# Optimization experiments

Measured on AMD Instinct MI355X. Metric: run time of the kernel, lower is better.

Reference implementation:

```python
import jax, jax.numpy as jnp
import numpy as np

B, T, D, U = 32, 512, 256, 1024

def setup_inputs() -> dict:
    key = jax.random.key(0)
    ks = jax.random.split(key, 5)
    return {
        "X_vecs": jax.random.normal(ks[0], (B, D), dtype=jnp.float32),
        "X_ts": jax.random.normal(ks[1], (B, T, D), dtype=jnp.float32),
        "mat_A_0": jax.random.normal(ks[2], (D, U), dtype=jnp.float32) * (1.0 / np.sqrt(D)),
        "vec_b_0": jnp.zeros((1, U), dtype=jnp.float32),
        "mat_A_s": jax.random.normal(ks[3], (D, U), dtype=jnp.float32) * (1.0 / np.sqrt(D)),
        "vec_b_s": jnp.zeros((1, U), dtype=jnp.float32),
        "mat_W_d": jax.random.normal(ks[4], (D, U), dtype=jnp.float32) * (1.0 / np.sqrt(D)),
        "vec_b_d": jnp.zeros((1, U), dtype=jnp.float32),
    }

def reference(X_vecs, X_ts, mat_A_0, vec_b_0, mat_A_s, vec_b_s, mat_W_d, vec_b_d):
    softsign = jax.nn.soft_sign  # x / (1 + |x|), the layer's main_activation
    # Learned initial state: H_0 = softsign(X_vecs @ A_0 + b_0)   [B, U]
    H0 = softsign(X_vecs @ mat_A_0 + vec_b_0)
    # Static per-step drive from the vector input (computed once, reused each t)
    drive = X_vecs @ mat_A_s + vec_b_s + vec_b_d  # [B, U]
    # Batched projection of the whole timeseries (one big GEMM instead of T small ones)
    XW = jnp.einsum('btd,du->btu', X_ts, mat_W_d)  # [B, T, U]
    def step(h, x_t):  # h: [B,U], x_t: [B,U]
        h_new = softsign(h + drive + x_t)
        return h_new, h_new
    _, outs = jax.lax.scan(step, H0, jnp.swapaxes(XW, 0, 1))  # outs: [T, B, U]
    return jnp.swapaxes(outs, 0, 1)  # return_sequences=True -> [B, T, U]
```

## Files before the change

kernel.cpp:

```cpp
#include <hip/hip_runtime.h>

#define B_DIM 32
#define T_DIM 512
#define D_DIM 256
#define U_DIM 1024
#define M_DIM (B_DIM * T_DIM)

typedef __bf16 bf16_t;
typedef bf16_t bf16x8 __attribute__((ext_vector_type(8)));
typedef float f32x4 __attribute__((ext_vector_type(4)));

__device__ __forceinline__ float ssign(float z) {
    return z * __builtin_amdgcn_rcpf(1.0f + __builtin_fabsf(z));
}

__global__ __launch_bounds__(256) void prep(const float* __restrict__ Wd,
                                            bf16_t* __restrict__ Wt,
                                            const float* __restrict__ X,
                                            bf16_t* __restrict__ Xb) {
    const int bid = blockIdx.x;
    if (bid < 64) {
        __shared__ float tile[64][65];
        const int tx = threadIdx.x & 63;
        const int ty = threadIdx.x >> 6;
        const int n0 = (bid & 15) * 64;
        const int k0 = (bid >> 4) * 64;
        #pragma unroll
        for (int rr = 0; rr < 16; ++rr) {
            const int kk = ty * 16 + rr;
            tile[kk][tx] = Wd[(size_t)(k0 + kk) * U_DIM + n0 + tx];
        }
        __syncthreads();
        #pragma unroll
        for (int rr = 0; rr < 16; ++rr) {
            const int nn = ty * 16 + rr;
            Wt[(size_t)(n0 + nn) * D_DIM + k0 + tx] = (bf16_t)tile[tx][nn];
        }
    } else {
        const int i = ((bid - 64) * 256 + threadIdx.x) * 8;
        const float4 a = *(const float4*)(X + i);
        const float4 b = *(const float4*)(X + i + 4);
        bf16x8 p;
        p[0]=(bf16_t)a.x; p[1]=(bf16_t)a.y; p[2]=(bf16_t)a.z; p[3]=(bf16_t)a.w;
        p[4]=(bf16_t)b.x; p[5]=(bf16_t)b.y; p[6]=(bf16_t)b.z; p[7]=(bf16_t)b.w;
        *(bf16x8*)(Xb + i) = p;
    }
}

__global__ __launch_bounds__(64, 1) void fused2(
        const float* __restrict__ Xv, const float* __restrict__ A0,
        const float* __restrict__ b0, const float* __restrict__ As,
        const float* __restrict__ bs, const float* __restrict__ bd,
        const bf16_t* __restrict__ Xb, const bf16_t* __restrict__ Wt,
        float* __restrict__ out) {
    __shared__ float xvs[D_DIM];
    __shared__ float xwT[2][64 * 20];

    const int lane = threadIdx.x;
    const int b = blockIdx.x;
    const int u0 = blockIdx.y * 64;
    const int lm = lane & 15, q = lane >> 4;
    const int u = u0 + lane;

    const bf16_t* xrow = Xb + ((size_t)b * T_DIM + lm) * D_DIM + q * 8;
    float* po = out + (size_t)b * T_DIM * U_DIM + u;

    bf16x8 aE[8], aO[8];
    #pragma unroll
    for (int kb = 0; kb < 8; ++kb) aE[kb] = *(const bf16x8*)(xrow + kb * 32);
    #pragma unroll
    for (int kb = 0; kb < 8; ++kb) aO[kb] = *(const bf16x8*)(xrow + (size_t)16 * D_DIM + kb * 32);

    bf16x8 bW[4][8];
    #pragma unroll
    for (int n = 0; n < 4; ++n)
        #pragma unroll
        for (int kb = 0; kb < 8; ++kb)
            bW[n][kb] = *(const bf16x8*)(Wt + (size_t)(u0 + n * 16 + lm) * D_DIM + kb * 32 + q * 8);

    ((float4*)xvs)[lane] = ((const float4*)(Xv + (size_t)b * D_DIM))[lane];
    __syncthreads();
    float h0a = 0.f, dra = 0.f;
    #pragma unroll 8
    for (int d = 0; d < D_DIM; ++d) {
        const float x = xvs[d];
        h0a = fmaf(x, A0[(size_t)d * U_DIM + u], h0a);
        dra = fmaf(x, As[(size_t)d * U_DIM + u], dra);
    }
    float h = ssign(h0a + b0[u]);
    const float drive = dra + bs[u] + bd[u];

#define DO_MFMA(ACC, AF)                                                            \
    {                                                                               \
        _Pragma("unroll")                                                           \
        for (int kb = 0; kb < 8; ++kb) {                                            \
            _Pragma("unroll")                                                       \
            for (int n = 0; n < 4; ++n)                                             \
                ACC[n] = __builtin_amdgcn_mfma_f32_16x16x32_bf16(AF[kb], bW[n][kb], \
                                                                 ACC[n], 0, 0, 0);  \
        }                                                                           \
    }

#define LOAD_A(DST, CH)                                                             \
    {                                                                               \
        const bf16_t* xp_ = xrow + (size_t)(CH) * 16 * D_DIM;                       \
        _Pragma("unroll")                                                           \
        for (int kb = 0; kb < 8; ++kb) DST[kb] = *(const bf16x8*)(xp_ + kb * 32);   \
    }

#define STASH(ACC, BUF)                                                             \
    {                                                                               \
        _Pragma("unroll")                                                           \
        for (int n = 0; n < 4; ++n)                                                 \
            *(f32x4*)&xwT[BUF][(n * 16 + lm) * 20 + q * 4] = ACC[n];                \
    }

#define SCAN16(BUF, CBASE)                                                          \
    {                                                                               \
        const f32x4 v0 = *(const f32x4*)&xwT[BUF][lane * 20 + 0];                   \
        const f32x4 v1 = *(const f32x4*)&xwT[BUF][lane * 20 + 4];                   \
        const f32x4 v2 = *(const f32x4*)&xwT[BUF][lane * 20 + 8];                   \
        const f32x4 v3 = *(const f32x4*)&xwT[BUF][lane * 20 + 12];                  \
        float xp[16];                                                               \
        _Pragma("unroll")                                                           \
        for (int r = 0; r < 4; ++r) {                                               \
            xp[r]      = drive + v0[r];                                             \
            xp[4 + r]  = drive + v1[r];                                             \
            xp[8 + r]  = drive + v2[r];                                             \
            xp[12 + r] = drive + v3[r];                                             \
        }                                                                           \
        _Pragma("unroll")                                                           \
        for (int j = 0; j < 16; ++j) {                                              \
            h = ssign(h + xp[j]);                                                   \
            po[(size_t)((CBASE) + j) * U_DIM] = h;                                  \
        }                                                                           \
    }

    f32x4 accC[4], accN[4];
    #pragma unroll
    for (int n = 0; n < 4; ++n) accC[n] = (f32x4){0.f, 0.f, 0.f, 0.f};
    DO_MFMA(accC, aE);

    for (int cc = 0; cc < 32; cc += 2) {
        STASH(accC, 0);
        #pragma unroll
        for (int n = 0; n < 4; ++n) accN[n] = (f32x4){0.f, 0.f, 0.f, 0.f};
        DO_MFMA(accN, aO);
        const int c2 = (cc + 2 < 32) ? cc + 2 : 31;
        LOAD_A(aE, c2);
        SCAN16(0, cc * 16);
        STASH(accN, 1);
        #pragma unroll
        for (int n = 0; n < 4; ++n) accC[n] = (f32x4){0.f, 0.f, 0.f, 0.f};
        DO_MFMA(accC, aE);
        const int c3 = (cc + 3 < 32) ? cc + 3 : 31;
        LOAD_A(aO, c3);
        SCAN16(1, (cc + 1) * 16);
    }
#undef DO_MFMA
#undef LOAD_A
#undef STASH
#undef SCAN16
}

__global__ __launch_bounds__(256) void gemm_xw_f32(const float* __restrict__ Xts,
                                                   const float* __restrict__ Wd,
                                                   float* __restrict__ out) {
    __shared__ float xs[16 * D_DIM];
    const int tid = threadIdx.x;
    const int bt0 = blockIdx.y * 16;
    const int u = blockIdx.x * 256 + tid;
    const float4* src4 = (const float4*)(Xts + (size_t)bt0 * D_DIM);
    float4* xs4 = (float4*)xs;
    #pragma unroll
    for (int i = 0; i < 4; ++i) xs4[tid + 256 * i] = src4[tid + 256 * i];
    __syncthreads();
    float acc[16];
    #pragma unroll
    for (int r = 0; r < 16; ++r) acc[r] = 0.0f;
    const float* wp = Wd + u;
    for (int d0 = 0; d0 < D_DIM; d0 += 4) {
        const float w0 = wp[(size_t)(d0 + 0) * U_DIM];
        const float w1 = wp[(size_t)(d0 + 1) * U_DIM];
        const float w2 = wp[(size_t)(d0 + 2) * U_DIM];
        const float w3 = wp[(size_t)(d0 + 3) * U_DIM];
        #pragma unroll
        for (int r = 0; r < 16; ++r) {
            const float4 xvv = *(const float4*)&xs[r * D_DIM + d0];
            acc[r] = fmaf(xvv.x, w0, acc[r]);
            acc[r] = fmaf(xvv.y, w1, acc[r]);
            acc[r] = fmaf(xvv.z, w2, acc[r]);
            acc[r] = fmaf(xvv.w, w3, acc[r]);
        }
    }
    #pragma unroll
    for (int r = 0; r < 16; ++r)
        out[(size_t)(bt0 + r) * U_DIM + u] = acc[r];
}

__global__ __launch_bounds__(256) void scan_old(const float* __restrict__ Xv,
                                                const float* __restrict__ A0,
                                                const float* __restrict__ b0,
                                                const float* __restrict__ As,
                                                const float* __restrict__ bs,
                                                const float* __restrict__ bd,
                                                float* __restrict__ out) {
    __shared__ float xv[D_DIM];
    const int tid = threadIdx.x;
    const int b = blockIdx.y;
    const int u = blockIdx.x * 256 + tid;
    xv[tid] = Xv[(size_t)b * D_DIM + tid];
    __syncthreads();
    float a0 = 0.0f, asum = 0.0f;
    #pragma unroll 4
    for (int d = 0; d < D_DIM; ++d) {
        const float x = xv[d];
        a0   = fmaf(x, A0[(size_t)d * U_DIM + u], a0);
        asum = fmaf(x, As[(size_t)d * U_DIM + u], asum);
    }
    a0 += b0[u];
    const float drive = asum + bs[u] + bd[u];
    float h = ssign(a0);
    float* po = out + (size_t)b * T_DIM * U_DIM + u;
    float buf[8];
    #pragma unroll
    for (int i = 0; i < 8; ++i) buf[i] = po[(size_t)i * U_DIM];
    for (int t = 0; t < T_DIM; t += 8) {
        #pragma unroll
        for (int i = 0; i < 8; ++i) {
            const float x = buf[i];
            const int tn = t + i + 8;
            if (tn < T_DIM) buf[i] = po[(size_t)tn * U_DIM];
            h = ssign(h + drive + x);
            po[(size_t)(t + i) * U_DIM] = h;
        }
    }
}

extern "C" void kernel_launch(void* const* d_in, const int* in_sizes, int n_in,
                              void* d_out, int out_size, void* d_ws, size_t ws_size,
                              hipStream_t stream) {
    const float* Xv  = (const float*)d_in[0];
    const float* Xts = (const float*)d_in[1];
    const float* A0  = (const float*)d_in[2];
    const float* b0  = (const float*)d_in[3];
    const float* As  = (const float*)d_in[4];
    const float* bs  = (const float*)d_in[5];
    const float* Wd  = (const float*)d_in[6];
    const float* bd  = (const float*)d_in[7];
    float* out = (float*)d_out;

    const size_t OFF_XB = 1u << 20;
    const size_t NEED   = 16u << 20;

    if (ws_size >= NEED) {
        bf16_t* Wt = (bf16_t*)d_ws;
        bf16_t* Xb = (bf16_t*)((char*)d_ws + OFF_XB);
        prep<<<dim3(64 + M_DIM * D_DIM / (256 * 8)), dim3(256), 0, stream>>>(Wd, Wt, Xts, Xb);
        fused2<<<dim3(B_DIM, U_DIM / 64), dim3(64), 0, stream>>>(
            Xv, A0, b0, As, bs, bd, Xb, Wt, out);
    } else {
        gemm_xw_f32<<<dim3(U_DIM / 256, M_DIM / 16), dim3(256), 0, stream>>>(Xts, Wd, out);
        scan_old<<<dim3(U_DIM / 256, B_DIM), dim3(256), 0, stream>>>(Xv, A0, b0, As, bs, bd, out);
    }
}
```

Baseline: 129.4 us.

## Warp-specialize fused kernel into MFMA producer and scan consumer waves

The fused kernel now runs two waves per block. One wave computes the X·W tiles with MFMA into a 4-slot shared-memory ring, and the other runs the sequential softsign scan and writes outputs, with barriers handing off between them. This aims to overlap the tensor-core work and the A-fragment loads with the latency-bound recurrence instead of interleaving them in one wave. The H0 and drive projections move into extra blocks of the prep kernel and go through workspace, so they no longer run serially at the start of each fused block. The cost is a barrier per 16-step chunk and an extra global round trip for H0 and drive.

```diff
diff --git a/kernel.cpp b/kernel.cpp
--- a/kernel.cpp
+++ b/kernel.cpp
@@ -17,7 +17,15 @@
 __global__ __launch_bounds__(256) void prep(const float* __restrict__ Wd,
                                             bf16_t* __restrict__ Wt,
                                             const float* __restrict__ X,
-                                            bf16_t* __restrict__ Xb) {
+                                            bf16_t* __restrict__ Xb,
+                                            const float* __restrict__ Xv,
+                                            const float* __restrict__ A0,
+                                            const float* __restrict__ b0,
+                                            const float* __restrict__ As,
+                                            const float* __restrict__ bs,
+                                            const float* __restrict__ bd,
+                                            float* __restrict__ H0o,
+                                            float* __restrict__ Dro) {
     const int bid = blockIdx.x;
     if (bid < 64) {
         __shared__ float tile[64][65];
@@ -36,7 +44,7 @@
             const int nn = ty * 16 + rr;
             Wt[(size_t)(n0 + nn) * D_DIM + k0 + tx] = (bf16_t)tile[tx][nn];
         }
-    } else {
+    } else if (bid < 2112) {
         const int i = ((bid - 64) * 256 + threadIdx.x) * 8;
         const float4 a = *(const float4*)(X + i);
         const float4 b = *(const float4*)(X + i + 4);
@@ -44,123 +52,149 @@
         p[0]=(bf16_t)a.x; p[1]=(bf16_t)a.y; p[2]=(bf16_t)a.z; p[3]=(bf16_t)a.w;
         p[4]=(bf16_t)b.x; p[5]=(bf16_t)b.y; p[6]=(bf16_t)b.z; p[7]=(bf16_t)b.w;
         *(bf16x8*)(Xb + i) = p;
-    }
-}
-
-__global__ __launch_bounds__(64, 1) void fused2(
-        const float* __restrict__ Xv, const float* __restrict__ A0,
-        const float* __restrict__ b0, const float* __restrict__ As,
-        const float* __restrict__ bs, const float* __restrict__ bd,
+    } else {
+        __shared__ float xv[D_DIM];
+        const int idx = bid - 2112;
+        const int b = idx >> 2;
+        const int u = (idx & 3) * 256 + threadIdx.x;
+        xv[threadIdx.x] = Xv[(size_t)b * D_DIM + threadIdx.x];
+        __syncthreads();
+        float a0 = 0.f, asum = 0.f;
+        #pragma unroll 8
+        for (int d = 0; d < D_DIM; ++d) {
+            const float x = xv[d];
+            a0   = fmaf(x, A0[(size_t)d * U_DIM + u], a0);
+            asum = fmaf(x, As[(size_t)d * U_DIM + u], asum);
+        }
+        H0o[(size_t)b * U_DIM + u] = ssign(a0 + b0[u]);
+        Dro[(size_t)b * U_DIM + u] = asum + bs[u] + bd[u];
+    }
+}
+
+__global__ __launch_bounds__(128, 1) void fused3(
+        const float* __restrict__ H0w, const float* __restrict__ Drw,
         const bf16_t* __restrict__ Xb, const bf16_t* __restrict__ Wt,
         float* __restrict__ out) {
-    __shared__ float xvs[D_DIM];
-    __shared__ float xwT[2][64 * 20];
-
-    const int lane = threadIdx.x;
+    __shared__ float xwT[4][64 * 20];
+
+    const int lane = threadIdx.x & 63;
+    const int wid = threadIdx.x >> 6;
     const int b = blockIdx.x;
     const int u0 = blockIdx.y * 64;
-    const int lm = lane & 15, q = lane >> 4;
-    const int u = u0 + lane;
-
-    const bf16_t* xrow = Xb + ((size_t)b * T_DIM + lm) * D_DIM + q * 8;
-    float* po = out + (size_t)b * T_DIM * U_DIM + u;
-
-    bf16x8 aE[8], aO[8];
-    #pragma unroll
-    for (int kb = 0; kb < 8; ++kb) aE[kb] = *(const bf16x8*)(xrow + kb * 32);
-    #pragma unroll
-    for (int kb = 0; kb < 8; ++kb) aO[kb] = *(const bf16x8*)(xrow + (size_t)16 * D_DIM + kb * 32);
-
-    bf16x8 bW[4][8];
-    #pragma unroll
-    for (int n = 0; n < 4; ++n)
-        #pragma unroll
-        for (int kb = 0; kb < 8; ++kb)
-            bW[n][kb] = *(const bf16x8*)(Wt + (size_t)(u0 + n * 16 + lm) * D_DIM + kb * 32 + q * 8);
-
-    ((float4*)xvs)[lane] = ((const float4*)(Xv + (size_t)b * D_DIM))[lane];
-    __syncthreads();
-    float h0a = 0.f, dra = 0.f;
-    #pragma unroll 8
-    for (int d = 0; d < D_DIM; ++d) {
-        const float x = xvs[d];
-        h0a = fmaf(x, A0[(size_t)d * U_DIM + u], h0a);
-        dra = fmaf(x, As[(size_t)d * U_DIM + u], dra);
-    }
-    float h = ssign(h0a + b0[u]);
-    const float drive = dra + bs[u] + bd[u];
-
-#define DO_MFMA(ACC, AF)                                                            \
+
+#define BARX()                                                          \
+    do {                                                                \
+        __asm__ volatile("s_waitcnt lgkmcnt(0)" ::: "memory");          \
+        __builtin_amdgcn_s_barrier();                                   \
+        __asm__ volatile("" ::: "memory");                              \
+    } while (0)
+
+    if (wid == 1) {
+        const int lm = lane & 15, q = lane >> 4;
+        const bf16_t* xrow = Xb + ((size_t)b * T_DIM + lm) * D_DIM + q * 8;
+
+#define LOADA(DST, CH)                                                              \
+    {                                                                               \
+        const bf16_t* xp_ = xrow + (size_t)(CH) * 16 * D_DIM;                       \
+        _Pragma("unroll")                                                           \
+        for (int kb = 0; kb < 8; ++kb) DST[kb] = *(const bf16x8*)(xp_ + kb * 32);   \
+    }
+
+        bf16x8 af0[8], af1[8], af2[8], af3[8];
+        LOADA(af0, 0); LOADA(af1, 1); LOADA(af2, 2); LOADA(af3, 3);
+
+        bf16x8 bW[4][8];
+        #pragma unroll
+        for (int n = 0; n < 4; ++n)
+            #pragma unroll
+            for (int kb = 0; kb < 8; ++kb)
+                bW[n][kb] = *(const bf16x8*)(Wt + (size_t)(u0 + n * 16 + lm) * D_DIM + kb * 32 + q * 8);
+
+        f32x4 acc[4];
+#define ZACC()                                                                      \
+    {                                                                               \
+        _Pragma("unroll")                                                           \
+        for (int n = 0; n < 4; ++n) acc[n] = (f32x4){0.f, 0.f, 0.f, 0.f};           \
+    }
+#define MM(AF)                                                                      \
     {                                                                               \
         _Pragma("unroll")                                                           \
         for (int kb = 0; kb < 8; ++kb) {                                            \
             _Pragma("unroll")                                                       \
             for (int n = 0; n < 4; ++n)                                             \
-                ACC[n] = __builtin_amdgcn_mfma_f32_16x16x32_bf16(AF[kb], bW[n][kb], \
-                                                                 ACC[n], 0, 0, 0);  \
+                acc[n] = __builtin_amdgcn_mfma_f32_16x16x32_bf16(AF[kb], bW[n][kb], \
+                                                                 acc[n], 0, 0, 0);  \
         }                                                                           \
     }
-
-#define LOAD_A(DST, CH)                                                             \
-    {                                                                               \
-        const bf16_t* xp_ = xrow + (size_t)(CH) * 16 * D_DIM;                       \
-        _Pragma("unroll")                                                           \
-        for (int kb = 0; kb < 8; ++kb) DST[kb] = *(const bf16x8*)(xp_ + kb * 32);   \
-    }
-
-#define STASH(ACC, BUF)                                                             \
+#define STASHS(SLOT)                                                                \
     {                                                                               \
         _Pragma("unroll")                                                           \
         for (int n = 0; n < 4; ++n)                                                 \
-            *(f32x4*)&xwT[BUF][(n * 16 + lm) * 20 + q * 4] = ACC[n];                \
-    }
-
-#define SCAN16(BUF, CBASE)                                                          \
-    {                                                                               \
-        const f32x4 v0 = *(const f32x4*)&xwT[BUF][lane * 20 + 0];                   \
-        const f32x4 v1 = *(const f32x4*)&xwT[BUF][lane * 20 + 4];                   \
-        const f32x4 v2 = *(const f32x4*)&xwT[BUF][lane * 20 + 8];                   \
-        const f32x4 v3 = *(const f32x4*)&xwT[BUF][lane * 20 + 12];                  \
-        float xp[16];                                                               \
-        _Pragma("unroll")                                                           \
-        for (int r = 0; r < 4; ++r) {                                               \
-            xp[r]      = drive + v0[r];                                             \
-            xp[4 + r]  = drive + v1[r];                                             \
-            xp[8 + r]  = drive + v2[r];                                             \
-            xp[12 + r] = drive + v3[r];                                             \
-        }                                                                           \
-        _Pragma("unroll")                                                           \
-        for (int j = 0; j < 16; ++j) {                                              \
-            h = ssign(h + xp[j]);                                                   \
-            po[(size_t)((CBASE) + j) * U_DIM] = h;                                  \
-        }                                                                           \
-    }
-
-    f32x4 accC[4], accN[4];
-    #pragma unroll
-    for (int n = 0; n < 4; ++n) accC[n] = (f32x4){0.f, 0.f, 0.f, 0.f};
-    DO_MFMA(accC, aE);
-
-    for (int cc = 0; cc < 32; cc += 2) {
-        STASH(accC, 0);
-        #pragma unroll
-        for (int n = 0; n < 4; ++n) accN[n] = (f32x4){0.f, 0.f, 0.f, 0.f};
-        DO_MFMA(accN, aO);
-        const int c2 = (cc + 2 < 32) ? cc + 2 : 31;
-        LOAD_A(aE, c2);
-        SCAN16(0, cc * 16);
-        STASH(accN, 1);
-        #pragma unroll
-        for (int n = 0; n < 4; ++n) accC[n] = (f32x4){0.f, 0.f, 0.f, 0.f};
-        DO_MFMA(accC, aE);
-        const int c3 = (cc + 3 < 32) ? cc + 3 : 31;
-        LOAD_A(aO, c3);
-        SCAN16(1, (cc + 1) * 16);
-    }
-#undef DO_MFMA
-#undef LOAD_A
-#undef STASH
-#undef SCAN16
+            *(f32x4*)&xwT[SLOT][(n * 16 + lm) * 20 + q * 4] = acc[n];               \
+    }
+
+        ZACC(); MM(af0); STASHS(0);
+        ZACC(); MM(af1); STASHS(1);
+        BARX();
+
+        #pragma unroll 1
+        for (int cc = 0; cc < 32; cc += 4) {
+            if (cc + 2 < 32) { if (cc + 4 < 32) LOADA(af0, cc + 4);
+                               ZACC(); MM(af2); STASHS(2); }
+            BARX();
+            if (cc + 3 < 32) { if (cc + 5 < 32) LOADA(af1, cc + 5);
+                               ZACC(); MM(af3); STASHS(3); }
+            BARX();
+            if (cc + 4 < 32) { if (cc + 6 < 32) LOADA(af2, cc + 6);
+                               ZACC(); MM(af0); STASHS(0); }
+            BARX();
+            if (cc + 5 < 32) { if (cc + 7 < 32) LOADA(af3, cc + 7);
+                               ZACC(); MM(af1); STASHS(1); }
+            BARX();
+        }
+#undef LOADA
+#undef ZACC
+#undef MM
+#undef STASHS
+    } else {
+        const int u = u0 + lane;
+        float h = H0w[(size_t)b * U_DIM + u];
+        const float drive = Drw[(size_t)b * U_DIM + u];
+        float* po = out + (size_t)b * T_DIM * U_DIM + u;
+
+        BARX();
+        const float* rb0 = &xwT[0][lane * 20];
+        f32x4 v0 = *(const f32x4*)(rb0 + 0);
+        f32x4 v1 = *(const f32x4*)(rb0 + 4);
+        f32x4 v2 = *(const f32x4*)(rb0 + 8);
+        f32x4 v3 = *(const f32x4*)(rb0 + 12);
+
+        #pragma unroll 1
+        for (int c = 0; c < 32; ++c) {
+            const float* rbn = &xwT[(c + 1) & 3][lane * 20];
+            f32x4 n0 = *(const f32x4*)(rbn + 0);
+            f32x4 n1 = *(const f32x4*)(rbn + 4);
+            f32x4 n2 = *(const f32x4*)(rbn + 8);
+            f32x4 n3 = *(const f32x4*)(rbn + 12);
+
+            float dv[16];
+            #pragma unroll
+            for (int r = 0; r < 4; ++r) {
+                dv[r]      = drive + v0[r];
+                dv[4 + r]  = drive + v1[r];
+                dv[8 + r]  = drive + v2[r];
+                dv[12 + r] = drive + v3[r];
+            }
+            #pragma unroll
+            for (int j = 0; j < 16; ++j) {
+                h = ssign(h + dv[j]);
+                po[(size_t)(c * 16 + j) * U_DIM] = h;
+            }
+            BARX();
+            v0 = n0; v1 = n1; v2 = n2; v3 = n3;
+        }
+    }
+#undef BARX
 }
 
 __global__ __launch_bounds__(256) void gemm_xw_f32(const float* __restrict__ Xts,
@@ -250,15 +284,19 @@
     const float* bd  = (const float*)d_in[7];
     float* out = (float*)d_out;
 
+    const size_t OFF_H0 = 512u << 10;
+    const size_t OFF_DR = 640u << 10;
     const size_t OFF_XB = 1u << 20;
     const size_t NEED   = 16u << 20;
 
     if (ws_size >= NEED) {
         bf16_t* Wt = (bf16_t*)d_ws;
+        float* H0w = (float*)((char*)d_ws + OFF_H0);
+        float* Drw = (float*)((char*)d_ws + OFF_DR);
         bf16_t* Xb = (bf16_t*)((char*)d_ws + OFF_XB);
-        prep<<<dim3(64 + M_DIM * D_DIM / (256 * 8)), dim3(256), 0, stream>>>(Wd, Wt, Xts, Xb);
-        fused2<<<dim3(B_DIM, U_DIM / 64), dim3(64), 0, stream>>>(
-            Xv, A0, b0, As, bs, bd, Xb, Wt, out);
+        prep<<<dim3(64 + M_DIM * D_DIM / (256 * 8) + 128), dim3(256), 0, stream>>>(
+            Wd, Wt, Xts, Xb, Xv, A0, b0, As, bs, bd, H0w, Drw);
+        fused3<<<dim3(B_DIM, U_DIM / 64), dim3(128), 0, stream>>>(H0w, Drw, Xb, Wt, out);
     } else {
         gemm_xw_f32<<<dim3(U_DIM / 256, M_DIM / 16), dim3(256), 0, stream>>>(Xts, Wd, out);
         scan_old<<<dim3(U_DIM / 256, B_DIM), dim3(256), 0, stream>>>(Xv, A0, b0, As, bs, bd, out);
```

After: 129.5 us. About the same (+0.0%).
